# Kernel optimization log

Hardware: AMD Instinct MI355X
Metric: run time of the kernel (lower is better)

The kernel has to match this reference:

```python
import jax, jax.numpy as jnp
import numpy as np

I, H, O, T = 512, 2048, 512, 4096

def setup_inputs() -> dict:
    key = jax.random.key(0)
    ks = jax.random.split(key, 7)
    s = 0.02  # small init scale to avoid gate saturation
    return {
        "input_seq": jax.random.normal(ks[0], (T, I), dtype=jnp.float32),
        "W_ih": jax.random.normal(ks[1], (4 * H, I), dtype=jnp.float32) * s,
        "W_hh": jax.random.normal(ks[2], (4 * H, H), dtype=jnp.float32) * s,
        "b_ih": jax.random.normal(ks[3], (4 * H,), dtype=jnp.float32) * s,
        "b_hh": jax.random.normal(ks[4], (4 * H,), dtype=jnp.float32) * s,
        "W_lin": jax.random.normal(ks[5], (O, H), dtype=jnp.float32) * s,
        "b_lin": jax.random.normal(ks[6], (O,), dtype=jnp.float32) * s,
    }

def reference(input_seq, W_ih, W_hh, b_ih, b_hh, W_lin, b_lin):
    # Single-layer LSTM, batch=1, initial (h, c) = 0; PyTorch gate order i,f,g,o.
    b = b_ih + b_hh
    # Precompute input projections for all timesteps: (T, 4H)
    xz = input_seq @ W_ih.T + b

    def step(carry, xz_t):
        h, c = carry
        z = xz_t + h @ W_hh.T  # (4H,)
        i, f, g, o = jnp.split(z, 4)
        i = jax.nn.sigmoid(i)
        f = jax.nn.sigmoid(f)
        g = jnp.tanh(g)
        o = jax.nn.sigmoid(o)
        c = f * c + i * g
        h = o * jnp.tanh(c)
        return (h, c), None

    h0 = jnp.zeros((H,), dtype=input_seq.dtype)
    c0 = jnp.zeros((H,), dtype=input_seq.dtype)
    (hT, _), _ = jax.lax.scan(step, (h0, c0), xz)
    # predictions[-1] == linear(lstm_out[-1]) == linear(h_T)
    return hT @ W_lin.T + b_lin
```

## Files before the change

### kernel.cpp

```cpp
#include <hip/hip_runtime.h>


#define TSTEPS 4096
#define HDIM   2048
#define GDIM   8192
#define IDIM   512
#define ODIM   512

#define XZ_BYTES ((size_t)TSTEPS * GDIM * sizeof(float))
#define FLAG_STRIDE 16

__device__ __forceinline__ float sigmoidf_fast(float x) {
    return 1.0f / (1.0f + __expf(-x));
}
__device__ __forceinline__ float tanhf_fast(float x) {
    return 2.0f / (1.0f + __expf(-2.0f * x)) - 1.0f;
}

__global__ __launch_bounds__(256) void xz_gemm(
    const float* __restrict__ A, const float* __restrict__ B,
    const float* __restrict__ bih, const float* __restrict__ bhh,
    float* __restrict__ C)
{
    __shared__ float As[16][132];
    __shared__ float Bs[16][132];

    const int tid = threadIdx.x;
    const int m0 = blockIdx.y * 128;
    const int n0 = blockIdx.x * 128;
    const int tx = tid & 15;
    const int ty = tid >> 4;

    const int lrow  = tid >> 1;
    const int kbase = (tid & 1) * 8;

    float acc[8][8] = {};

    for (int k0 = 0; k0 < IDIM; k0 += 16) {
        const float4 av0 = *(const float4*)(A + (size_t)(m0 + lrow) * IDIM + k0 + kbase);
        const float4 av1 = *(const float4*)(A + (size_t)(m0 + lrow) * IDIM + k0 + kbase + 4);
        const float4 bv0 = *(const float4*)(B + (size_t)(n0 + lrow) * IDIM + k0 + kbase);
        const float4 bv1 = *(const float4*)(B + (size_t)(n0 + lrow) * IDIM + k0 + kbase + 4);

        __syncthreads();
        As[kbase + 0][lrow] = av0.x; As[kbase + 1][lrow] = av0.y;
        As[kbase + 2][lrow] = av0.z; As[kbase + 3][lrow] = av0.w;
        As[kbase + 4][lrow] = av1.x; As[kbase + 5][lrow] = av1.y;
        As[kbase + 6][lrow] = av1.z; As[kbase + 7][lrow] = av1.w;
        Bs[kbase + 0][lrow] = bv0.x; Bs[kbase + 1][lrow] = bv0.y;
        Bs[kbase + 2][lrow] = bv0.z; Bs[kbase + 3][lrow] = bv0.w;
        Bs[kbase + 4][lrow] = bv1.x; Bs[kbase + 5][lrow] = bv1.y;
        Bs[kbase + 6][lrow] = bv1.z; Bs[kbase + 7][lrow] = bv1.w;
        __syncthreads();

#pragma unroll
        for (int kk = 0; kk < 16; ++kk) {
            const float4 a0 = *(const float4*)&As[kk][ty * 8];
            const float4 a1 = *(const float4*)&As[kk][ty * 8 + 4];
            const float4 b0 = *(const float4*)&Bs[kk][tx * 8];
            const float4 b1 = *(const float4*)&Bs[kk][tx * 8 + 4];
            const float ar[8] = {a0.x, a0.y, a0.z, a0.w, a1.x, a1.y, a1.z, a1.w};
            const float br[8] = {b0.x, b0.y, b0.z, b0.w, b1.x, b1.y, b1.z, b1.w};
#pragma unroll
            for (int i = 0; i < 8; ++i)
#pragma unroll
                for (int jj = 0; jj < 8; ++jj)
                    acc[i][jj] = fmaf(ar[i], br[jj], acc[i][jj]);
        }
    }

    float bias[8];
#pragma unroll
    for (int jj = 0; jj < 8; ++jj) {
        const int n = n0 + tx * 8 + jj;
        bias[jj] = bih[n] + bhh[n];
    }
#pragma unroll
    for (int i = 0; i < 8; ++i) {
        float* crow = C + (size_t)(m0 + ty * 8 + i) * GDIM + n0 + tx * 8;
        float4 v0, v1;
        v0.x = acc[i][0] + bias[0]; v0.y = acc[i][1] + bias[1];
        v0.z = acc[i][2] + bias[2]; v0.w = acc[i][3] + bias[3];
        v1.x = acc[i][4] + bias[4]; v1.y = acc[i][5] + bias[5];
        v1.z = acc[i][6] + bias[6]; v1.w = acc[i][7] + bias[7];
        ((float4*)crow)[0] = v0;
        ((float4*)crow)[1] = v1;
    }
}

__global__ __launch_bounds__(256, 1) void lstm_rec(
    const float* __restrict__ Whh, const float* __restrict__ xz,
    float* __restrict__ hbuf, unsigned* __restrict__ flags)
{
    __shared__ float hsh[8 * 260];

    const int tidb = threadIdx.x;
    const int tid  = blockIdx.x * 256 + tidb;
    const int j    = tid >> 5;
    const int g    = (tid >> 3) & 3;
    const int ck   = tid & 7;
    const int row  = g * HDIM + j;
    const int wv   = tidb >> 6;
    const int ln   = tidb & 63;

    const float4* wsrc = (const float4*)(Whh + (size_t)row * HDIM + ck * 256);
    float4 w[64];
#pragma unroll
    for (int i = 0; i < 64; ++i) w[i] = wsrc[i];

    const bool owner = (tid & 31) == 0;
    float cstate = 0.0f;

    const unsigned* myflag = flags + (size_t)(wv * 64 + ln) * FLAG_STRIDE;

    float zx = xz[row];

    for (int t = 0; t < TSTEPS; ++t) {
        {
            const unsigned need = (unsigned)t;
            unsigned spins = 0;
            while (__hip_atomic_load(myflag, __ATOMIC_RELAXED,
                                     __HIP_MEMORY_SCOPE_AGENT) < need) {
                __builtin_amdgcn_s_sleep(1);
                if (++spins > (1u << 22)) break;
            }
        }

        const float* hsrc = hbuf + ((t & 1) << 11) + wv * 512;
        float hv[8];
#pragma unroll
        for (int m = 0; m < 8; ++m)
            hv[m] = __hip_atomic_load(hsrc + m * 64 + ln, __ATOMIC_RELAXED,
                                      __HIP_MEMORY_SCOPE_AGENT);
#pragma unroll
        for (int m = 0; m < 8; ++m) {
            const int k = wv * 512 + m * 64 + ln;
            hsh[(k >> 8) * 260 + (k & 255)] = hv[m];
        }
        __syncthreads();

        const float4* hr = (const float4*)(hsh + ck * 260);
        float a0 = 0.f, a1 = 0.f, a2 = 0.f, a3 = 0.f;
#pragma unroll
        for (int i = 0; i < 64; ++i) {
            const float4 h4 = hr[i];
            a0 = fmaf(w[i].x, h4.x, a0);
            a1 = fmaf(w[i].y, h4.y, a1);
            a2 = fmaf(w[i].z, h4.z, a2);
            a3 = fmaf(w[i].w, h4.w, a3);
        }
        float d = (a0 + a1) + (a2 + a3);
        d += __shfl_xor(d, 1);
        d += __shfl_xor(d, 2);
        d += __shfl_xor(d, 4);
        const float z  = d + zx;
        const float zf = __shfl_xor(z, 8);
        const float zg = __shfl_xor(z, 16);
        const float zo = __shfl_xor(z, 24);

        if (owner) {
            const float ig = sigmoidf_fast(z);
            const float fg = sigmoidf_fast(zf);
            const float gg = tanhf_fast(zg);
            const float og = sigmoidf_fast(zo);
            cstate = fmaf(fg, cstate, ig * gg);
            const float hval = og * tanhf_fast(cstate);
            __hip_atomic_store(hbuf + (((t + 1) & 1) << 11) + j, hval,
                               __ATOMIC_RELAXED, __HIP_MEMORY_SCOPE_AGENT);
        }

        const int tn = (t + 1 < TSTEPS) ? (t + 1) : (TSTEPS - 1);
        zx = xz[(size_t)tn * GDIM + row];

        __syncthreads();
        if (tidb == 0)
            __hip_atomic_store(flags + (size_t)blockIdx.x * FLAG_STRIDE,
                               (unsigned)(t + 1), __ATOMIC_RELAXED,
                               __HIP_MEMORY_SCOPE_AGENT);
    }
}

__global__ __launch_bounds__(256) void final_linear(
    const float* __restrict__ Wlin, const float* __restrict__ blin,
    const float* __restrict__ hT, float* __restrict__ out)
{
    const int wid  = (blockIdx.x * 256 + threadIdx.x) >> 6;
    const int lane = threadIdx.x & 63;
    const float4* wr = (const float4*)(Wlin + (size_t)wid * HDIM);
    const float4* hp = (const float4*)hT;
    float acc = 0.f;
#pragma unroll
    for (int i = 0; i < 8; ++i) {
        const float4 w4 = wr[lane + 64 * i];
        const float4 h4 = hp[lane + 64 * i];
        acc += w4.x * h4.x + w4.y * h4.y + w4.z * h4.z + w4.w * h4.w;
    }
#pragma unroll
    for (int off = 32; off > 0; off >>= 1) acc += __shfl_down(acc, off);
    if (lane == 0) out[wid] = acc + blin[wid];
}

extern "C" void kernel_launch(void* const* d_in, const int* in_sizes, int n_in,
                              void* d_out, int out_size, void* d_ws, size_t ws_size,
                              hipStream_t stream) {
    const float* input = (const float*)d_in[0];
    const float* Wih   = (const float*)d_in[1];
    const float* Whh   = (const float*)d_in[2];
    const float* bih   = (const float*)d_in[3];
    const float* bhh   = (const float*)d_in[4];
    const float* Wlin  = (const float*)d_in[5];
    const float* blin  = (const float*)d_in[6];
    float* out = (float*)d_out;

    char* ws = (char*)d_ws;
    float*    xz    = (float*)ws;
    float*    hbuf  = (float*)(ws + XZ_BYTES);
    unsigned* flags = (unsigned*)(ws + XZ_BYTES + 2 * HDIM * sizeof(float));

    hipMemsetAsync(hbuf, 0,
                   2 * HDIM * sizeof(float) + 256 * FLAG_STRIDE * sizeof(unsigned),
                   stream);

    dim3 ggrid(GDIM / 128, TSTEPS / 128);
    xz_gemm<<<ggrid, 256, 0, stream>>>(input, Wih, bih, bhh, xz);

    lstm_rec<<<dim3(256), dim3(256), 0, stream>>>(Whh, xz, hbuf, flags);

    final_linear<<<ODIM / 4, 256, 0, stream>>>(Wlin, blin, hbuf, out);
}
```

Measured before the change: 17.85 ms.

## Pack h values with step tags into 16-byte lines to remove separate flags

The per-block flag plus separate h-buffer handshake is replaced by 16-byte lines that each carry two h values together with their timestep tags. Consumers poll the data lines directly with uncached vector loads until every tag matches, then write the values into a double-buffered LDS area. This removes the trailing __syncthreads and the flag store, and hoists the next xz load ahead of the dot product. It relies on 16-byte stores being seen atomically by other CUs, and it shortens the spin timeout after the first one expires.

```diff
diff --git a/kernel.cpp b/kernel.cpp
--- a/kernel.cpp
+++ b/kernel.cpp
@@ -8,13 +8,34 @@
 #define ODIM   512
 
 #define XZ_BYTES ((size_t)TSTEPS * GDIM * sizeof(float))
-#define FLAG_STRIDE 16
+
+typedef int int4v __attribute__((ext_vector_type(4)));
 
 __device__ __forceinline__ float sigmoidf_fast(float x) {
     return 1.0f / (1.0f + __expf(-x));
 }
 __device__ __forceinline__ float tanhf_fast(float x) {
     return 2.0f / (1.0f + __expf(-2.0f * x)) - 1.0f;
+}
+
+__device__ __forceinline__ void poll4(const int4v* p0, const int4v* p1,
+                                      const int4v* p2, const int4v* p3,
+                                      int4v& a, int4v& b, int4v& c, int4v& d)
+{
+    asm volatile(
+        "global_load_dwordx4 %0, %4, off sc0 sc1\n\t"
+        "global_load_dwordx4 %1, %5, off sc0 sc1\n\t"
+        "global_load_dwordx4 %2, %6, off sc0 sc1\n\t"
+        "global_load_dwordx4 %3, %7, off sc0 sc1\n\t"
+        "s_waitcnt vmcnt(0)"
+        : "=&v"(a), "=&v"(b), "=&v"(c), "=&v"(d)
+        : "v"(p0), "v"(p1), "v"(p2), "v"(p3)
+        : "memory");
+}
+__device__ __forceinline__ void store_line(int4v* p, int4v v)
+{
+    asm volatile("global_store_dwordx4 %0, %1, off sc0 sc1"
+                 :: "v"(p), "v"(v) : "memory");
 }
 
 __global__ __launch_bounds__(256) void xz_gemm(
@@ -90,9 +111,9 @@
 
 __global__ __launch_bounds__(256, 1) void lstm_rec(
     const float* __restrict__ Whh, const float* __restrict__ xz,
-    float* __restrict__ hbuf, unsigned* __restrict__ flags)
-{
-    __shared__ float hsh[8 * 260];
+    int4v* __restrict__ lines)
+{
+    __shared__ float hsh[2 * 2080];
 
     const int tidb = threadIdx.x;
     const int tid  = blockIdx.x * 256 + tidb;
@@ -111,35 +132,47 @@
     const bool owner = (tid & 31) == 0;
     float cstate = 0.0f;
 
-    const unsigned* myflag = flags + (size_t)(wv * 64 + ln) * FLAG_STRIDE;
+    int4v*       sl0 = lines + (blockIdx.x * 4 + wv);
+    int4v*       sl1 = sl0 + 1024;
+    const int4v* cb0 = lines + 256 * wv + ln;
+    const int4v* cb1 = cb0 + 1024;
 
     float zx = xz[row];
 
+    unsigned cap = 1u << 21;
+
     for (int t = 0; t < TSTEPS; ++t) {
+        int4v v0, v1, v2, v3;
         {
             const unsigned need = (unsigned)t;
+            const int4v* cb = (t & 1) ? cb1 : cb0;
             unsigned spins = 0;
-            while (__hip_atomic_load(myflag, __ATOMIC_RELAXED,
-                                     __HIP_MEMORY_SCOPE_AGENT) < need) {
+            for (;;) {
+                poll4(cb, cb + 64, cb + 128, cb + 192, v0, v1, v2, v3);
+                const bool ok =
+                    ((unsigned)v0.y >= need) & ((unsigned)v0.w >= need) &
+                    ((unsigned)v1.y >= need) & ((unsigned)v1.w >= need) &
+                    ((unsigned)v2.y >= need) & ((unsigned)v2.w >= need) &
+                    ((unsigned)v3.y >= need) & ((unsigned)v3.w >= need);
+                if (ok) break;
                 __builtin_amdgcn_s_sleep(1);
-                if (++spins > (1u << 22)) break;
+                if (++spins > cap) { cap = 2048; break; }
             }
         }
 
-        const float* hsrc = hbuf + ((t & 1) << 11) + wv * 512;
-        float hv[8];
-#pragma unroll
-        for (int m = 0; m < 8; ++m)
-            hv[m] = __hip_atomic_load(hsrc + m * 64 + ln, __ATOMIC_RELAXED,
-                                      __HIP_MEMORY_SCOPE_AGENT);
-#pragma unroll
-        for (int m = 0; m < 8; ++m) {
-            const int k = wv * 512 + m * 64 + ln;
-            hsh[(k >> 8) * 260 + (k & 255)] = hv[m];
-        }
+        const int buf = t & 1;
+        const int b0  = buf * 2080 + (2 * wv) * 260;
+        const int b1  = b0 + 260;
+        *(float2*)&hsh[b0 +       2 * ln] = make_float2(__int_as_float(v0.x), __int_as_float(v0.z));
+        *(float2*)&hsh[b0 + 128 + 2 * ln] = make_float2(__int_as_float(v1.x), __int_as_float(v1.z));
+        *(float2*)&hsh[b1 +       2 * ln] = make_float2(__int_as_float(v2.x), __int_as_float(v2.z));
+        *(float2*)&hsh[b1 + 128 + 2 * ln] = make_float2(__int_as_float(v3.x), __int_as_float(v3.z));
         __syncthreads();
 
-        const float4* hr = (const float4*)(hsh + ck * 260);
+        const int tn = (t + 1 < TSTEPS) ? (t + 1) : (TSTEPS - 1);
+        const float zx_next = xz[(size_t)tn * GDIM + row];
+
+        const float4* hr = (const float4*)(hsh + buf * 2080 + ck * 260);
         float a0 = 0.f, a1 = 0.f, a2 = 0.f, a3 = 0.f;
 #pragma unroll
         for (int i = 0; i < 64; ++i) {
@@ -158,42 +191,42 @@
         const float zg = __shfl_xor(z, 16);
         const float zo = __shfl_xor(z, 24);
 
+        float hval = 0.0f;
         if (owner) {
             const float ig = sigmoidf_fast(z);
             const float fg = sigmoidf_fast(zf);
             const float gg = tanhf_fast(zg);
             const float og = sigmoidf_fast(zo);
             cstate = fmaf(fg, cstate, ig * gg);
-            const float hval = og * tanhf_fast(cstate);
-            __hip_atomic_store(hbuf + (((t + 1) & 1) << 11) + j, hval,
-                               __ATOMIC_RELAXED, __HIP_MEMORY_SCOPE_AGENT);
-        }
-
-        const int tn = (t + 1 < TSTEPS) ? (t + 1) : (TSTEPS - 1);
-        zx = xz[(size_t)tn * GDIM + row];
-
-        __syncthreads();
-        if (tidb == 0)
-            __hip_atomic_store(flags + (size_t)blockIdx.x * FLAG_STRIDE,
-                               (unsigned)(t + 1), __ATOMIC_RELAXED,
-                               __HIP_MEMORY_SCOPE_AGENT);
+            hval = og * tanhf_fast(cstate);
+        }
+        const float h1 = __shfl(hval, 32);
+        if (ln == 0) {
+            int4v sv;
+            sv.x = __float_as_int(hval); sv.y = t + 1;
+            sv.z = __float_as_int(h1);   sv.w = t + 1;
+            store_line(((t + 1) & 1) ? sl1 : sl0, sv);
+        }
+        zx = zx_next;
     }
 }
 
 __global__ __launch_bounds__(256) void final_linear(
     const float* __restrict__ Wlin, const float* __restrict__ blin,
-    const float* __restrict__ hT, float* __restrict__ out)
+    const int4v* __restrict__ hl, float* __restrict__ out)
 {
     const int wid  = (blockIdx.x * 256 + threadIdx.x) >> 6;
     const int lane = threadIdx.x & 63;
     const float4* wr = (const float4*)(Wlin + (size_t)wid * HDIM);
-    const float4* hp = (const float4*)hT;
     float acc = 0.f;
 #pragma unroll
     for (int i = 0; i < 8; ++i) {
-        const float4 w4 = wr[lane + 64 * i];
-        const float4 h4 = hp[lane + 64 * i];
-        acc += w4.x * h4.x + w4.y * h4.y + w4.z * h4.z + w4.w * h4.w;
+        const int k = lane + 64 * i;
+        const float4 w4 = wr[k];
+        const int4v la = hl[2 * k];
+        const int4v lb = hl[2 * k + 1];
+        acc += w4.x * __int_as_float(la.x) + w4.y * __int_as_float(la.z)
+             + w4.z * __int_as_float(lb.x) + w4.w * __int_as_float(lb.z);
     }
 #pragma unroll
     for (int off = 32; off > 0; off >>= 1) acc += __shfl_down(acc, off);
@@ -213,18 +246,15 @@
     float* out = (float*)d_out;
 
     char* ws = (char*)d_ws;
-    float*    xz    = (float*)ws;
-    float*    hbuf  = (float*)(ws + XZ_BYTES);
-    unsigned* flags = (unsigned*)(ws + XZ_BYTES + 2 * HDIM * sizeof(float));
-
-    hipMemsetAsync(hbuf, 0,
-                   2 * HDIM * sizeof(float) + 256 * FLAG_STRIDE * sizeof(unsigned),
-                   stream);
+    float* xz    = (float*)ws;
+    int4v* lines = (int4v*)(ws + XZ_BYTES);
+
+    hipMemsetAsync(lines, 0, 2 * 1024 * sizeof(int4v), stream);
 
     dim3 ggrid(GDIM / 128, TSTEPS / 128);
     xz_gemm<<<ggrid, 256, 0, stream>>>(input, Wih, bih, bhh, xz);
 
-    lstm_rec<<<dim3(256), dim3(256), 0, stream>>>(Whh, xz, hbuf, flags);
-
-    final_linear<<<ODIM / 4, 256, 0, stream>>>(Wlin, blin, hbuf, out);
-}
+    lstm_rec<<<dim3(256), dim3(256), 0, stream>>>(Whh, xz, lines);
+
+    final_linear<<<ODIM / 4, 256, 0, stream>>>(Wlin, blin, lines, out);
+}
```

After: 16.37 ms. 1.09x faster.
